# Optimization experiments

Measured on AMD Instinct MI355X. Metric: run time of the kernel, lower is better.

Reference implementation:

```python
import jax, jax.numpy as jnp
import numpy as np

N_P, N_A = 200_000, 100_000
D_P, D_A, H, OUT = 64, 64, 32, 1
E_PP, E_AP, E_PA = 3_200_000, 1_600_000, 1_600_000


def _lin(key, din, dout, bias=True):
    kw, kb = jax.random.split(key)
    W = jax.random.normal(kw, (din, dout), jnp.float32) * (1.0 / np.sqrt(din))
    if bias:
        b = jax.random.normal(kb, (dout,), jnp.float32) * 0.01
        return W, b
    return W


def setup_inputs() -> dict:
    key = jax.random.key(0)
    ks = jax.random.split(key, 24)
    inp = {}
    inp['x_paper'] = jax.random.normal(ks[0], (N_P, D_P), jnp.float32)
    inp['x_author'] = jax.random.normal(ks[1], (N_A, D_A), jnp.float32)
    inp['src_pp'] = jax.random.randint(ks[2], (E_PP,), 0, N_P)
    inp['dst_pp'] = jax.random.randint(ks[3], (E_PP,), 0, N_P)
    inp['src_ap'] = jax.random.randint(ks[4], (E_AP,), 0, N_A)
    inp['dst_ap'] = jax.random.randint(ks[5], (E_AP,), 0, N_P)
    inp['src_pa'] = jax.random.randint(ks[6], (E_PA,), 0, N_P)
    inp['dst_pa'] = jax.random.randint(ks[7], (E_PA,), 0, N_A)
    # Layer-1 SAGEConv weights per relation: lin_l (neighbor, with bias), lin_r (root, no bias)
    inp['Wl1_pp'], inp['bl1_pp'] = _lin(ks[8], D_P, H)
    inp['Wr1_pp'] = _lin(ks[9], D_P, H, bias=False)
    inp['Wl1_ap'], inp['bl1_ap'] = _lin(ks[10], D_A, H)
    inp['Wr1_ap'] = _lin(ks[11], D_P, H, bias=False)
    inp['Wl1_pa'], inp['bl1_pa'] = _lin(ks[12], D_P, H)
    inp['Wr1_pa'] = _lin(ks[13], D_A, H, bias=False)
    # Layer-2 SAGEConv weights (only relations feeding 'paper' affect the output)
    inp['Wl2_pp'], inp['bl2_pp'] = _lin(ks[14], H, H)
    inp['Wr2_pp'] = _lin(ks[15], H, H, bias=False)
    inp['Wl2_ap'], inp['bl2_ap'] = _lin(ks[16], H, H)
    inp['Wr2_ap'] = _lin(ks[17], H, H, bias=False)
    # Final classifier Linear(32, 1)
    inp['W_lin'], inp['b_lin'] = _lin(ks[18], H, OUT)
    return inp


def _sage_rel(x_src, x_dst, src, dst, Wl, bl, Wr):
    # SAGEConv: lin_l(mean_{j in N(i)} x_j) + lin_r(x_i)
    n_dst = x_dst.shape[0]
    agg = jax.ops.segment_sum(x_src[src], dst, num_segments=n_dst)
    cnt = jax.ops.segment_sum(jnp.ones((src.shape[0],), x_src.dtype), dst, num_segments=n_dst)
    mean = agg / jnp.maximum(cnt, 1.0)[:, None]
    return mean @ Wl + bl + x_dst @ Wr


def reference(x_paper, x_author, src_pp, dst_pp, src_ap, dst_ap, src_pa, dst_pa,
              Wl1_pp, bl1_pp, Wr1_pp, Wl1_ap, bl1_ap, Wr1_ap, Wl1_pa, bl1_pa, Wr1_pa,
              Wl2_pp, bl2_pp, Wr2_pp, Wl2_ap, bl2_ap, Wr2_ap, W_lin, b_lin):
    # Layer 1 (to_hetero: sum per-relation conv outputs per destination type), then relu
    p1 = (_sage_rel(x_paper, x_paper, src_pp, dst_pp, Wl1_pp, bl1_pp, Wr1_pp)
          + _sage_rel(x_author, x_paper, src_ap, dst_ap, Wl1_ap, bl1_ap, Wr1_ap))
    a1 = _sage_rel(x_paper, x_author, src_pa, dst_pa, Wl1_pa, bl1_pa, Wr1_pa)
    p1, a1 = jax.nn.relu(p1), jax.nn.relu(a1)
    # Layer 2: only 'paper' output is consumed downstream
    p2 = (_sage_rel(p1, p1, src_pp, dst_pp, Wl2_pp, bl2_pp, Wr2_pp)
          + _sage_rel(a1, p1, src_ap, dst_ap, Wl2_ap, bl2_ap, Wr2_ap))
    # model_config is None -> plain Linear, no sigmoid/softmax
    return p2 @ W_lin + b_lin
```

## Files before the change

kernel.cpp:

```cpp
#include <hip/hip_runtime.h>


typedef unsigned short ushort_t;
typedef __attribute__((ext_vector_type(8))) short bf16x8;
typedef __attribute__((ext_vector_type(4))) float f32x4;

#define PWBITS 9
#define PWIN   (1 << PWBITS)
#define PCHUNK 4096
#define CAPPAD 2048
#define FW_R   12

__device__ inline ushort_t f2bf(float f) {
    unsigned u = __float_as_uint(f);
    unsigned r = (u + 0x7FFFu + ((u >> 16) & 1u)) >> 16;
    return (ushort_t)r;
}
__device__ inline float bf2f_lo(unsigned u) { return __uint_as_float(u << 16); }
__device__ inline float bf2f_hi(unsigned u) { return __uint_as_float(u & 0xFFFF0000u); }
__device__ inline int ntl(const int* p) { return __builtin_nontemporal_load(p); }

__global__ void prep_weights(
    const float* __restrict__ Wl1_pp, const float* __restrict__ Wr1_pp,
    const float* __restrict__ Wl1_ap, const float* __restrict__ Wr1_ap,
    const float* __restrict__ Wl1_pa, const float* __restrict__ Wr1_pa,
    const float* __restrict__ bl1_pp, const float* __restrict__ bl1_ap,
    const float* __restrict__ bl1_pa,
    const float* __restrict__ Wl2_pp, const float* __restrict__ bl2_pp,
    const float* __restrict__ Wr2_pp,
    const float* __restrict__ Wl2_ap, const float* __restrict__ bl2_ap,
    const float* __restrict__ Wr2_ap,
    const float* __restrict__ W_lin, const float* __restrict__ b_lin,
    float* __restrict__ Wcomb_p,
    float* __restrict__ Wcomb_a,
    ushort_t* __restrict__ Wfrag_p,
    ushort_t* __restrict__ Wfrag_a,
    float* __restrict__ bias_p,
    float* __restrict__ bias_a,
    float* __restrict__ vv)
{
    int t = threadIdx.x;
    for (int idx = t; idx < 64 * 96; idx += 256) {
        int i = idx / 96, j = idx % 96;
        float v;
        if (j < 32)       v = Wl1_pp[i * 32 + j];
        else if (j < 64)  v = Wl1_pa[i * 32 + (j - 32)];
        else              v = Wr1_pp[i * 32 + (j - 64)] + Wr1_ap[i * 32 + (j - 64)];
        Wcomb_p[idx] = v;
    }
    for (int idx = t; idx < 64 * 64; idx += 256) {
        int i = idx / 64, j = idx % 64;
        Wcomb_a[idx] = (j < 32) ? Wl1_ap[i * 32 + j] : Wr1_pa[i * 32 + (j - 32)];
    }
    if (t < 32) {
        bias_p[t] = bl1_pp[t] + bl1_ap[t];
        bias_a[t] = bl1_pa[t];
        float vpp = 0.f, vr = 0.f, vap = 0.f;
        for (int j = 0; j < 32; ++j) {
            float wl = W_lin[j];
            vpp += Wl2_pp[t * 32 + j] * wl;
            vr  += (Wr2_pp[t * 32 + j] + Wr2_ap[t * 32 + j]) * wl;
            vap += Wl2_ap[t * 32 + j] * wl;
        }
        vv[t] = vpp; vv[32 + t] = vr; vv[96 + t] = vap;
    }
    if (t == 0) {
        float c = b_lin[0];
        for (int j = 0; j < 32; ++j) c += (bl2_pp[j] + bl2_ap[j]) * W_lin[j];
        vv[64] = c;
    }
    __syncthreads();
    for (int idx = t; idx < 12 * 64 * 8; idx += 256) {
        int f = idx >> 9, l = (idx >> 3) & 63, j = idx & 7;
        int nt = f >> 1, kh = f & 1;
        int k = kh * 32 + 8 * (l >> 4) + j;
        int n = nt * 16 + (l & 15);
        Wfrag_p[idx] = f2bf(Wcomb_p[k * 96 + n]);
    }
    for (int idx = t; idx < 8 * 64 * 8; idx += 256) {
        int f = idx >> 9, l = (idx >> 3) & 63, j = idx & 7;
        int nt = f >> 1, kh = f & 1;
        int k = kh * 32 + 8 * (l >> 4) + j;
        int n = nt * 16 + (l & 15);
        Wfrag_a[idx] = f2bf(Wcomb_a[k * 64 + n]);
    }
}

__global__ __launch_bounds__(256)
void partition3(
    const int* __restrict__ src0, const int* __restrict__ dst0, int E0,
    unsigned* __restrict__ bk0, int cap0, int nw0, int* __restrict__ wc0,
    const int* __restrict__ src1, const int* __restrict__ dst1, int E1,
    unsigned* __restrict__ bk1, int cap1, int nw1, int* __restrict__ wc1,
    const int* __restrict__ src2, const int* __restrict__ dst2, int E2,
    unsigned* __restrict__ bk2, int cap2, int nw2, int* __restrict__ wc2)
{
    __shared__ int lcnt[PWIN];
    __shared__ int lbase[PWIN];
    int nb0 = (E0 + PCHUNK - 1) / PCHUNK;
    int nb1 = (E1 + PCHUNK - 1) / PCHUNK;
    int b = blockIdx.x;
    const int* src; const int* dst; int E; unsigned* bk; int cap; int nw; int* wc; int chunk;
    if (b < nb0)            { src = src0; dst = dst0; E = E0; bk = bk0; cap = cap0; nw = nw0; wc = wc0; chunk = b; }
    else if (b < nb0 + nb1) { src = src1; dst = dst1; E = E1; bk = bk1; cap = cap1; nw = nw1; wc = wc1; chunk = b - nb0; }
    else                    { src = src2; dst = dst2; E = E2; bk = bk2; cap = cap2; nw = nw2; wc = wc2; chunk = b - nb0 - nb1; }
    int e0 = chunk * PCHUNK;
    int d_[16], s_[16];
#pragma unroll
    for (int r = 0; r < 4; ++r) {
        int base = e0 + r * 1024 + threadIdx.x * 4;
        if (base + 3 < E) {
            int4 dv = *(const int4*)(dst + base);
            int4 sv = *(const int4*)(src + base);
            d_[r * 4 + 0] = dv.x; d_[r * 4 + 1] = dv.y; d_[r * 4 + 2] = dv.z; d_[r * 4 + 3] = dv.w;
            s_[r * 4 + 0] = sv.x; s_[r * 4 + 1] = sv.y; s_[r * 4 + 2] = sv.z; s_[r * 4 + 3] = sv.w;
        } else {
#pragma unroll
            for (int k = 0; k < 4; ++k) {
                int e = base + k;
                d_[r * 4 + k] = (e < E) ? dst[e] : -1;
                s_[r * 4 + k] = 0;
            }
        }
    }
    for (int i = threadIdx.x; i < nw; i += 256) lcnt[i] = 0;
    __syncthreads();
#pragma unroll
    for (int k = 0; k < 16; ++k)
        if (d_[k] >= 0) atomicAdd(&lcnt[((unsigned)d_[k]) >> PWBITS], 1);
    __syncthreads();
    for (int i = threadIdx.x; i < nw; i += 256) {
        int c = lcnt[i];
        lbase[i] = (c > 0) ? atomicAdd(&wc[i * 16], c) : 0;
        lcnt[i] = 0;
    }
    __syncthreads();
#pragma unroll
    for (int k = 0; k < 16; ++k) {
        int d = d_[k];
        if (d >= 0) {
            int w = ((unsigned)d) >> PWBITS;
            int off = lbase[w] + atomicAdd(&lcnt[w], 1);
            if (off < cap)
                bk[(size_t)w * cap + off] =
                    (((unsigned)(d & (PWIN - 1))) << 18) | (unsigned)s_[k];
        }
    }
}

__global__ __launch_bounds__(256)
void fill_win3(
    const unsigned* __restrict__ bk0, const int* __restrict__ wc0, int cap0,
    int* __restrict__ csr0, int* __restrict__ cnt0, int* __restrict__ rs0, int N0, int nw0,
    const unsigned* __restrict__ bk1, const int* __restrict__ wc1, int cap1,
    int* __restrict__ csr1, int* __restrict__ cnt1, int* __restrict__ rs1, int N1, int nw1,
    const unsigned* __restrict__ bk2, const int* __restrict__ wc2, int cap2,
    int* __restrict__ csr2, int* __restrict__ cnt2, int* __restrict__ rs2, int N2, int nw2)
{
    __shared__ int lc[PWIN];
    __shared__ int wsum[4], wpre[4];
    int b = blockIdx.x;
    const unsigned* bk; const int* wc; int cap; int* csr; int* cnt; int* rs; int N; int w;
    if (b < nw0)            { bk = bk0; wc = wc0; cap = cap0; csr = csr0; cnt = cnt0; rs = rs0; N = N0; w = b; }
    else if (b < nw0 + nw1) { bk = bk1; wc = wc1; cap = cap1; csr = csr1; cnt = cnt1; rs = rs1; N = N1; w = b - nw0; }
    else                    { bk = bk2; wc = wc2; cap = cap2; csr = csr2; cnt = cnt2; rs = rs2; N = N2; w = b - nw0 - nw1; }
    int d0 = w << PWBITS;
    int sz = wc[w * 16]; if (sz > cap) sz = cap;
    const unsigned* bkt = bk + (size_t)w * cap;
    uint4 u[FW_R];
#pragma unroll
    for (int r = 0; r < FW_R; ++r) {
        int i4 = r * 1024 + threadIdx.x * 4;
        if (i4 + 3 < sz) {
            u[r] = *(const uint4*)(bkt + i4);
        } else {
            u[r].x = (i4 + 0 < sz) ? bkt[i4 + 0] : 0xFFFFFFFFu;
            u[r].y = (i4 + 1 < sz) ? bkt[i4 + 1] : 0xFFFFFFFFu;
            u[r].z = (i4 + 2 < sz) ? bkt[i4 + 2] : 0xFFFFFFFFu;
            u[r].w = (i4 + 3 < sz) ? bkt[i4 + 3] : 0xFFFFFFFFu;
        }
    }
    for (int i = threadIdx.x; i < PWIN; i += 256) lc[i] = 0;
    __syncthreads();
#pragma unroll
    for (int r = 0; r < FW_R; ++r) {
        if (u[r].x != 0xFFFFFFFFu) atomicAdd(&lc[u[r].x >> 18], 1);
        if (u[r].y != 0xFFFFFFFFu) atomicAdd(&lc[u[r].y >> 18], 1);
        if (u[r].z != 0xFFFFFFFFu) atomicAdd(&lc[u[r].z >> 18], 1);
        if (u[r].w != 0xFFFFFFFFu) atomicAdd(&lc[u[r].w >> 18], 1);
    }
    __syncthreads();
    {
        int i = threadIdx.x * 2;
        int d = d0 + i;
        if (d < N)     cnt[d] = lc[i];
        if (d + 1 < N) cnt[d + 1] = lc[i + 1];
    }
    int t2 = threadIdx.x * 2;
    int v0 = lc[t2], v1 = lc[t2 + 1];
    int ts = v0 + v1;
    int lane = threadIdx.x & 63;
    int wid = threadIdx.x >> 6;
    int incl = ts;
#pragma unroll
    for (int off = 1; off < 64; off <<= 1) {
        int o = __shfl_up(incl, off);
        if (lane >= off) incl += o;
    }
    if (lane == 63) wsum[wid] = incl;
    __syncthreads();
    if (threadIdx.x == 0) {
        int r = 0;
        for (int i = 0; i < 4; ++i) { wpre[i] = r; r += wsum[i]; }
    }
    __syncthreads();
    int run = w * cap + wpre[wid] + (incl - ts);
    lc[t2] = run;
    if (d0 + t2 < N) rs[d0 + t2] = run;
    run += v0;
    lc[t2 + 1] = run;
    if (d0 + t2 + 1 < N) rs[d0 + t2 + 1] = run;
    __syncthreads();
#pragma unroll
    for (int r = 0; r < FW_R; ++r) {
        if (u[r].x != 0xFFFFFFFFu) { int p = atomicAdd(&lc[u[r].x >> 18], 1); csr[p] = (int)(u[r].x & 0x3FFFFu); }
        if (u[r].y != 0xFFFFFFFFu) { int p = atomicAdd(&lc[u[r].y >> 18], 1); csr[p] = (int)(u[r].y & 0x3FFFFu); }
        if (u[r].z != 0xFFFFFFFFu) { int p = atomicAdd(&lc[u[r].z >> 18], 1); csr[p] = (int)(u[r].z & 0x3FFFFu); }
        if (u[r].w != 0xFFFFFFFFu) { int p = atomicAdd(&lc[u[r].w >> 18], 1); csr[p] = (int)(u[r].w & 0x3FFFFu); }
    }
}

__device__ inline bf16x8 cvt8(const float* p) {
    float4 a = *(const float4*)p;
    float4 b = *(const float4*)(p + 4);
    bf16x8 r;
    r[0] = (short)f2bf(a.x); r[1] = (short)f2bf(a.y);
    r[2] = (short)f2bf(a.z); r[3] = (short)f2bf(a.w);
    r[4] = (short)f2bf(b.x); r[5] = (short)f2bf(b.y);
    r[6] = (short)f2bf(b.z); r[7] = (short)f2bf(b.w);
    return r;
}

__global__ __launch_bounds__(256)
void proj_paper_mfma(const float* __restrict__ x, const ushort_t* __restrict__ Wfrag,
                     const float* __restrict__ bias,
                     ushort_t* __restrict__ h_pp, ushort_t* __restrict__ h_pa,
                     float* __restrict__ root_p, int N)
{
    int wave = threadIdx.x >> 6, lane = threadIdx.x & 63;
    int mbase = blockIdx.x * 64 + wave * 16;
    int row = lane & 15, grp = lane >> 4;
    int nA = mbase + row; if (nA > N - 1) nA = N - 1;
    const float* xr = x + (size_t)nA * 64 + grp * 8;
    bf16x8 a0 = cvt8(xr);
    bf16x8 a1 = cvt8(xr + 32);
    f32x4 acc0 = {0.f, 0.f, 0.f, 0.f}, acc1 = acc0, acc2 = acc0, acc3 = acc0;
    float bp0 = bias[row];
    float bp1 = bias[16 + row];
    f32x4 acc4 = {bp0, bp0, bp0, bp0};
    f32x4 acc5 = {bp1, bp1, bp1, bp1};
    const bf16x8* wf = (const bf16x8*)(Wfrag) + lane;
    acc0 = __builtin_amdgcn_mfma_f32_16x16x32_bf16(a0, wf[0 * 64], acc0, 0, 0, 0);
    acc0 = __builtin_amdgcn_mfma_f32_16x16x32_bf16(a1, wf[1 * 64], acc0, 0, 0, 0);
    acc1 = __builtin_amdgcn_mfma_f32_16x16x32_bf16(a0, wf[2 * 64], acc1, 0, 0, 0);
    acc1 = __builtin_amdgcn_mfma_f32_16x16x32_bf16(a1, wf[3 * 64], acc1, 0, 0, 0);
    acc2 = __builtin_amdgcn_mfma_f32_16x16x32_bf16(a0, wf[4 * 64], acc2, 0, 0, 0);
    acc2 = __builtin_amdgcn_mfma_f32_16x16x32_bf16(a1, wf[5 * 64], acc2, 0, 0, 0);
    acc3 = __builtin_amdgcn_mfma_f32_16x16x32_bf16(a0, wf[6 * 64], acc3, 0, 0, 0);
    acc3 = __builtin_amdgcn_mfma_f32_16x16x32_bf16(a1, wf[7 * 64], acc3, 0, 0, 0);
    acc4 = __builtin_amdgcn_mfma_f32_16x16x32_bf16(a0, wf[8 * 64], acc4, 0, 0, 0);
    acc4 = __builtin_amdgcn_mfma_f32_16x16x32_bf16(a1, wf[9 * 64], acc4, 0, 0, 0);
    acc5 = __builtin_amdgcn_mfma_f32_16x16x32_bf16(a0, wf[10 * 64], acc5, 0, 0, 0);
    acc5 = __builtin_amdgcn_mfma_f32_16x16x32_bf16(a1, wf[11 * 64], acc5, 0, 0, 0);
    int col = row;
    int node0 = mbase + grp * 4;
#pragma unroll
    for (int reg = 0; reg < 4; ++reg) {
        int nd = node0 + reg;
        if (nd < N) {
            size_t b32 = (size_t)nd * 32;
            h_pp[b32 + col]        = f2bf(acc0[reg]);
            h_pp[b32 + 16 + col]   = f2bf(acc1[reg]);
            h_pa[b32 + col]        = f2bf(acc2[reg]);
            h_pa[b32 + 16 + col]   = f2bf(acc3[reg]);
            root_p[b32 + col]      = acc4[reg];
            root_p[b32 + 16 + col] = acc5[reg];
        }
    }
}

__global__ __launch_bounds__(256)
void proj_author_mfma(const float* __restrict__ x, const ushort_t* __restrict__ Wfrag,
                      const float* __restrict__ bias,
                      ushort_t* __restrict__ h_ap, float* __restrict__ root_a, int N)
{
    int wave = threadIdx.x >> 6, lane = threadIdx.x & 63;
    int mbase = blockIdx.x * 64 + wave * 16;
    int row = lane & 15, grp = lane >> 4;
    int nA = mbase + row; if (nA > N - 1) nA = N - 1;
    const float* xr = x + (size_t)nA * 64 + grp * 8;
    bf16x8 a0 = cvt8(xr);
    bf16x8 a1 = cvt8(xr + 32);
    f32x4 acc0 = {0.f, 0.f, 0.f, 0.f}, acc1 = acc0;
    float bp0 = bias[row];
    float bp1 = bias[16 + row];
    f32x4 acc2 = {bp0, bp0, bp0, bp0};
    f32x4 acc3 = {bp1, bp1, bp1, bp1};
    const bf16x8* wf = (const bf16x8*)(Wfrag) + lane;
    acc0 = __builtin_amdgcn_mfma_f32_16x16x32_bf16(a0, wf[0 * 64], acc0, 0, 0, 0);
    acc0 = __builtin_amdgcn_mfma_f32_16x16x32_bf16(a1, wf[1 * 64], acc0, 0, 0, 0);
    acc1 = __builtin_amdgcn_mfma_f32_16x16x32_bf16(a0, wf[2 * 64], acc1, 0, 0, 0);
    acc1 = __builtin_amdgcn_mfma_f32_16x16x32_bf16(a1, wf[3 * 64], acc1, 0, 0, 0);
    acc2 = __builtin_amdgcn_mfma_f32_16x16x32_bf16(a0, wf[4 * 64], acc2, 0, 0, 0);
    acc2 = __builtin_amdgcn_mfma_f32_16x16x32_bf16(a1, wf[5 * 64], acc2, 0, 0, 0);
    acc3 = __builtin_amdgcn_mfma_f32_16x16x32_bf16(a0, wf[6 * 64], acc3, 0, 0, 0);
    acc3 = __builtin_amdgcn_mfma_f32_16x16x32_bf16(a1, wf[7 * 64], acc3, 0, 0, 0);
    int col = row;
    int node0 = mbase + grp * 4;
#pragma unroll
    for (int reg = 0; reg < 4; ++reg) {
        int nd = node0 + reg;
        if (nd < N) {
            size_t b32 = (size_t)nd * 32;
            h_ap[b32 + col]        = f2bf(acc0[reg]);
            h_ap[b32 + 16 + col]   = f2bf(acc1[reg]);
            root_a[b32 + col]      = acc2[reg];
            root_a[b32 + 16 + col] = acc3[reg];
        }
    }
}

#define ACC8(A, U) \
    A[0] += bf2f_lo((U).x); A[1] += bf2f_hi((U).x); \
    A[2] += bf2f_lo((U).y); A[3] += bf2f_hi((U).y); \
    A[4] += bf2f_lo((U).z); A[5] += bf2f_hi((U).z); \
    A[6] += bf2f_lo((U).w); A[7] += bf2f_hi((U).w);

__global__ __launch_bounds__(256, 8)
void pull_paper(const ushort_t* __restrict__ h_pp, const ushort_t* __restrict__ h_ap,
                const float* __restrict__ root,
                const int* __restrict__ csr_pp, const int* __restrict__ rs_pp,
                const int* __restrict__ cnt_pp,
                const int* __restrict__ csr_ap, const int* __restrict__ rs_ap,
                const int* __restrict__ cnt_ap,
                const float* __restrict__ vv,
                float* __restrict__ s_pp, float* __restrict__ out, int N)
{
    __shared__ float v0[32], v1[32];
    __shared__ float c2s;
    if (threadIdx.x < 32) { v0[threadIdx.x] = vv[threadIdx.x]; v1[threadIdx.x] = vv[32 + threadIdx.x]; }
    if (threadIdx.x == 0) c2s = vv[64];
    __syncthreads();
    int n = blockIdx.x * 64 + (threadIdx.x >> 2);
    if (n >= N) return;
    int c = threadIdx.x & 3;
    float a[8];
#pragma unroll
    for (int k = 0; k < 8; ++k) a[k] = 0.f;
    int s1 = rs_pp[n], k1 = cnt_pp[n], e1 = s1 + k1;
    int j = s1;
    for (; j + 4 <= e1; j += 4) {
        int i0 = ntl(csr_pp + j), i1 = ntl(csr_pp + j + 1);
        int i2 = ntl(csr_pp + j + 2), i3 = ntl(csr_pp + j + 3);
        uint4 u0 = ((const uint4*)(h_pp + (size_t)i0 * 32))[c];
        uint4 u1 = ((const uint4*)(h_pp + (size_t)i1 * 32))[c];
        uint4 u2 = ((const uint4*)(h_pp + (size_t)i2 * 32))[c];
        uint4 u3 = ((const uint4*)(h_pp + (size_t)i3 * 32))[c];
        ACC8(a, u0) ACC8(a, u1) ACC8(a, u2) ACC8(a, u3)
    }
    for (; j < e1; ++j) {
        uint4 u0 = ((const uint4*)(h_pp + (size_t)ntl(csr_pp + j) * 32))[c];
        ACC8(a, u0)
    }
    float b[8];
#pragma unroll
    for (int k = 0; k < 8; ++k) b[k] = 0.f;
    int s2 = rs_ap[n], k2 = cnt_ap[n], e2 = s2 + k2;
    j = s2;
    for (; j + 4 <= e2; j += 4) {
        int i0 = ntl(csr_ap + j), i1 = ntl(csr_ap + j + 1);
        int i2 = ntl(csr_ap + j + 2), i3 = ntl(csr_ap + j + 3);
        uint4 u0 = ((const uint4*)(h_ap + (size_t)i0 * 32))[c];
        uint4 u1 = ((const uint4*)(h_ap + (size_t)i1 * 32))[c];
        uint4 u2 = ((const uint4*)(h_ap + (size_t)i2 * 32))[c];
        uint4 u3 = ((const uint4*)(h_ap + (size_t)i3 * 32))[c];
        ACC8(b, u0) ACC8(b, u1) ACC8(b, u2) ACC8(b, u3)
    }
    for (; j < e2; ++j) {
        uint4 u0 = ((const uint4*)(h_ap + (size_t)ntl(csr_ap + j) * 32))[c];
        ACC8(b, u0)
    }
    float ipp = 1.0f / fmaxf((float)k1, 1.0f);
    float iap = 1.0f / fmaxf((float)k2, 1.0f);
    const float* rt = root + (size_t)n * 32 + 8 * c;
    float d0 = 0.f, d1 = 0.f;
#pragma unroll
    for (int k = 0; k < 8; ++k) {
        float p = fmaxf(rt[k] + a[k] * ipp + b[k] * iap, 0.f);
        d0 += p * v0[8 * c + k];
        d1 += p * v1[8 * c + k];
    }
    d0 += __shfl_xor(d0, 1); d0 += __shfl_xor(d0, 2);
    d1 += __shfl_xor(d1, 1); d1 += __shfl_xor(d1, 2);
    if (c == 0) { s_pp[n] = d0; out[n] = d1 + c2s; }
}

__global__ __launch_bounds__(256, 8)
void pull_author(const ushort_t* __restrict__ h_pa, const float* __restrict__ root,
                 const int* __restrict__ csr_pa, const int* __restrict__ rs_pa,
                 const int* __restrict__ cnt_pa,
                 const float* __restrict__ vv, float* __restrict__ s_ap, int N)
{
    __shared__ float v0[32];
    if (threadIdx.x < 32) v0[threadIdx.x] = vv[96 + threadIdx.x];
    __syncthreads();
    int n = blockIdx.x * 64 + (threadIdx.x >> 2);
    if (n >= N) return;
    int c = threadIdx.x & 3;
    float a[8];
#pragma unroll
    for (int k = 0; k < 8; ++k) a[k] = 0.f;
    int s1 = rs_pa[n], k1 = cnt_pa[n], e1 = s1 + k1;
    int j = s1;
    for (; j + 4 <= e1; j += 4) {
        int i0 = ntl(csr_pa + j), i1 = ntl(csr_pa + j + 1);
        int i2 = ntl(csr_pa + j + 2), i3 = ntl(csr_pa + j + 3);
        uint4 u0 = ((const uint4*)(h_pa + (size_t)i0 * 32))[c];
        uint4 u1 = ((const uint4*)(h_pa + (size_t)i1 * 32))[c];
        uint4 u2 = ((const uint4*)(h_pa + (size_t)i2 * 32))[c];
        uint4 u3 = ((const uint4*)(h_pa + (size_t)i3 * 32))[c];
        ACC8(a, u0) ACC8(a, u1) ACC8(a, u2) ACC8(a, u3)
    }
    for (; j < e1; ++j) {
        uint4 u0 = ((const uint4*)(h_pa + (size_t)ntl(csr_pa + j) * 32))[c];
        ACC8(a, u0)
    }
    float ip = 1.0f / fmaxf((float)k1, 1.0f);
    const float* rt = root + (size_t)n * 32 + 8 * c;
    float d0 = 0.f;
#pragma unroll
    for (int k = 0; k < 8; ++k) {
        float p = fmaxf(rt[k] + a[k] * ip, 0.f);
        d0 += p * v0[8 * c + k];
    }
    d0 += __shfl_xor(d0, 1); d0 += __shfl_xor(d0, 2);
    if (c == 0) s_ap[n] = d0;
}

__global__ __launch_bounds__(256, 8)
void pull2(const float* __restrict__ s_pp, const float* __restrict__ s_ap,
           const int* __restrict__ csr_pp, const int* __restrict__ rs_pp,
           const int* __restrict__ cnt_pp,
           const int* __restrict__ csr_ap, const int* __restrict__ rs_ap,
           const int* __restrict__ cnt_ap,
           float* __restrict__ out, int N)
{
    int g = (blockIdx.x * blockDim.x + threadIdx.x) >> 2;
    int c = threadIdx.x & 3;
    if (g >= N) return;
    int s1 = rs_pp[g], k1 = cnt_pp[g], e1 = s1 + k1;
    float t = 0.f;
    for (int j = s1 + c; j < e1; j += 4) t += s_pp[ntl(csr_pp + j)];
    int s2 = rs_ap[g], k2 = cnt_ap[g], e2 = s2 + k2;
    float u = 0.f;
    for (int j = s2 + c; j < e2; j += 4) u += s_ap[ntl(csr_ap + j)];
    t += __shfl_xor(t, 1); t += __shfl_xor(t, 2);
    u += __shfl_xor(u, 1); u += __shfl_xor(u, 2);
    if (c == 0) {
        out[g] += t / fmaxf((float)k1, 1.f) + u / fmaxf((float)k2, 1.f);
    }
}

extern "C" void kernel_launch(void* const* d_in, const int* in_sizes, int n_in,
                              void* d_out, int out_size, void* d_ws, size_t ws_size,
                              hipStream_t stream)
{
    const float* x_paper  = (const float*)d_in[0];
    const float* x_author = (const float*)d_in[1];
    const int* src_pp = (const int*)d_in[2];
    const int* dst_pp = (const int*)d_in[3];
    const int* src_ap = (const int*)d_in[4];
    const int* dst_ap = (const int*)d_in[5];
    const int* src_pa = (const int*)d_in[6];
    const int* dst_pa = (const int*)d_in[7];
    const float* Wl1_pp = (const float*)d_in[8];
    const float* bl1_pp = (const float*)d_in[9];
    const float* Wr1_pp = (const float*)d_in[10];
    const float* Wl1_ap = (const float*)d_in[11];
    const float* bl1_ap = (const float*)d_in[12];
    const float* Wr1_ap = (const float*)d_in[13];
    const float* Wl1_pa = (const float*)d_in[14];
    const float* bl1_pa = (const float*)d_in[15];
    const float* Wr1_pa = (const float*)d_in[16];
    const float* Wl2_pp = (const float*)d_in[17];
    const float* bl2_pp = (const float*)d_in[18];
    const float* Wr2_pp = (const float*)d_in[19];
    const float* Wl2_ap = (const float*)d_in[20];
    const float* bl2_ap = (const float*)d_in[21];
    const float* Wr2_ap = (const float*)d_in[22];
    const float* W_lin  = (const float*)d_in[23];
    const float* b_lin  = (const float*)d_in[24];

    const int NP = in_sizes[0] / 64;
    const int NA = in_sizes[1] / 64;
    const int E_PP = in_sizes[2];
    const int E_AP = in_sizes[4];
    const int E_PA = in_sizes[6];

    const int nw_pp = (NP + PWIN - 1) >> PWBITS;
    const int nw_ap = nw_pp;
    const int nw_pa = (NA + PWIN - 1) >> PWBITS;
    const int cap_pp = ((E_PP / nw_pp + CAPPAD) + 3) & ~3;
    const int cap_ap = ((E_AP / nw_ap + CAPPAD) + 3) & ~3;
    const int cap_pa = ((E_PA / nw_pa + CAPPAD) + 3) & ~3;

    char* wp = (char*)d_ws;
    int* wcur = (int*)wp;             wp += (size_t)3 * PWIN * 16 * 4;
    unsigned* bk_pp = (unsigned*)wp;  wp += (size_t)nw_pp * cap_pp * 4;
    unsigned* bk_ap = (unsigned*)wp;  wp += (size_t)nw_ap * cap_ap * 4;
    unsigned* bk_pa = (unsigned*)wp;  wp += (size_t)nw_pa * cap_pa * 4;
    int* csr_pp = (int*)wp;           wp += (size_t)nw_pp * cap_pp * 4;
    int* csr_ap = (int*)wp;           wp += (size_t)nw_ap * cap_ap * 4;
    int* csr_pa = (int*)wp;           wp += (size_t)nw_pa * cap_pa * 4;
    int* cnt    = (int*)wp;           wp += (size_t)(2 * NP + NA) * 4;
    int* rs     = (int*)wp;           wp += (size_t)(2 * NP + NA) * 4;
    ushort_t* h_pp = (ushort_t*)wp;   wp += (size_t)NP * 32 * 2;
    ushort_t* h_pa = (ushort_t*)wp;   wp += (size_t)NP * 32 * 2;
    ushort_t* h_ap = (ushort_t*)wp;   wp += (size_t)NA * 32 * 2;
    float* root_a = (float*)wp;       wp += (size_t)NA * 32 * 4;
    float* s_pp   = (float*)wp;       wp += (size_t)NP * 4;
    float* s_ap   = (float*)wp;       wp += (size_t)NA * 4;
    float* Wcomb_p = (float*)wp;      wp += 64 * 96 * 4;
    float* Wcomb_a = (float*)wp;      wp += 64 * 64 * 4;
    ushort_t* Wfrag_p = (ushort_t*)wp; wp += 12 * 64 * 8 * 2;
    ushort_t* Wfrag_a = (ushort_t*)wp; wp += 8 * 64 * 8 * 2;
    float* bias_p = (float*)wp;       wp += 32 * 4;
    float* bias_a = (float*)wp;       wp += 32 * 4;
    float* vv     = (float*)wp;       wp += 128 * 4;
    float* root_p = (float*)bk_pp;

    int* cnt_pp = cnt,  * cnt_ap = cnt + NP,  * cnt_pa = cnt + 2 * NP;
    int* rs_pp  = rs,   * rs_ap  = rs + NP,   * rs_pa  = rs + 2 * NP;

    float* out = (float*)d_out;

    hipMemsetAsync(wcur, 0, (size_t)3 * PWIN * 16 * 4, stream);

    prep_weights<<<1, 256, 0, stream>>>(
        Wl1_pp, Wr1_pp, Wl1_ap, Wr1_ap, Wl1_pa, Wr1_pa,
        bl1_pp, bl1_ap, bl1_pa,
        Wl2_pp, bl2_pp, Wr2_pp, Wl2_ap, bl2_ap, Wr2_ap,
        W_lin, b_lin, Wcomb_p, Wcomb_a, Wfrag_p, Wfrag_a, bias_p, bias_a, vv);

    int nb_total = (E_PP + PCHUNK - 1) / PCHUNK + (E_AP + PCHUNK - 1) / PCHUNK
                 + (E_PA + PCHUNK - 1) / PCHUNK;
    partition3<<<nb_total, 256, 0, stream>>>(
        src_pp, dst_pp, E_PP, bk_pp, cap_pp, nw_pp, wcur + 0,
        src_ap, dst_ap, E_AP, bk_ap, cap_ap, nw_ap, wcur + PWIN * 16,
        src_pa, dst_pa, E_PA, bk_pa, cap_pa, nw_pa, wcur + 2 * PWIN * 16);

    fill_win3<<<nw_pp + nw_ap + nw_pa, 256, 0, stream>>>(
        bk_pp, wcur + 0,            cap_pp, csr_pp, cnt_pp, rs_pp, NP, nw_pp,
        bk_ap, wcur + PWIN * 16,    cap_ap, csr_ap, cnt_ap, rs_ap, NP, nw_ap,
        bk_pa, wcur + 2 * PWIN * 16, cap_pa, csr_pa, cnt_pa, rs_pa, NA, nw_pa);

    proj_paper_mfma<<<(NP + 63) / 64, 256, 0, stream>>>(
        x_paper, Wfrag_p, bias_p, h_pp, h_pa, root_p, NP);
    proj_author_mfma<<<(NA + 63) / 64, 256, 0, stream>>>(
        x_author, Wfrag_a, bias_a, h_ap, root_a, NA);

    pull_paper<<<(NP + 63) / 64, 256, 0, stream>>>(
        h_pp, h_ap, root_p, csr_pp, rs_pp, cnt_pp, csr_ap, rs_ap, cnt_ap,
        vv, s_pp, out, NP);
    pull_author<<<(NA + 63) / 64, 256, 0, stream>>>(
        h_pa, root_a, csr_pa, rs_pa, cnt_pa, vv, s_ap, NA);

    pull2<<<((size_t)NP * 4 + 255) / 256, 256, 0, stream>>>(
        s_pp, s_ap, csr_pp, rs_pp, cnt_pp, csr_ap, rs_ap, cnt_ap, out, NP);
}
```

Measured before the change: 375.6 us.

## Fuse edge partition with node projection kernels into a single launch

```diff
diff --git a/kernel.cpp b/kernel.cpp
--- a/kernel.cpp
+++ b/kernel.cpp
@@ -31,12 +31,9 @@
     const float* __restrict__ Wl2_ap, const float* __restrict__ bl2_ap,
     const float* __restrict__ Wr2_ap,
     const float* __restrict__ W_lin, const float* __restrict__ b_lin,
-    float* __restrict__ Wcomb_p,
-    float* __restrict__ Wcomb_a,
-    ushort_t* __restrict__ Wfrag_p,
-    ushort_t* __restrict__ Wfrag_a,
-    float* __restrict__ bias_p,
-    float* __restrict__ bias_a,
+    float* __restrict__ Wcomb_p, float* __restrict__ Wcomb_a,
+    ushort_t* __restrict__ Wfrag_p, ushort_t* __restrict__ Wfrag_a,
+    float* __restrict__ bias_p, float* __restrict__ bias_a,
     float* __restrict__ vv)
 {
     int t = threadIdx.x;
@@ -86,20 +83,16 @@
     }
 }
 
-__global__ __launch_bounds__(256)
-void partition3(
+__device__ inline void partition_body(
+    int b, int nb0, int nb1,
     const int* __restrict__ src0, const int* __restrict__ dst0, int E0,
     unsigned* __restrict__ bk0, int cap0, int nw0, int* __restrict__ wc0,
     const int* __restrict__ src1, const int* __restrict__ dst1, int E1,
     unsigned* __restrict__ bk1, int cap1, int nw1, int* __restrict__ wc1,
     const int* __restrict__ src2, const int* __restrict__ dst2, int E2,
-    unsigned* __restrict__ bk2, int cap2, int nw2, int* __restrict__ wc2)
-{
-    __shared__ int lcnt[PWIN];
-    __shared__ int lbase[PWIN];
-    int nb0 = (E0 + PCHUNK - 1) / PCHUNK;
-    int nb1 = (E1 + PCHUNK - 1) / PCHUNK;
-    int b = blockIdx.x;
+    unsigned* __restrict__ bk2, int cap2, int nw2, int* __restrict__ wc2,
+    int* lcnt, int* lbase)
+{
     const int* src; const int* dst; int E; unsigned* bk; int cap; int nw; int* wc; int chunk;
     if (b < nb0)            { src = src0; dst = dst0; E = E0; bk = bk0; cap = cap0; nw = nw0; wc = wc0; chunk = b; }
     else if (b < nb0 + nb1) { src = src1; dst = dst1; E = E1; bk = bk1; cap = cap1; nw = nw1; wc = wc1; chunk = b - nb0; }
@@ -148,88 +141,6 @@
     }
 }
 
-__global__ __launch_bounds__(256)
-void fill_win3(
-    const unsigned* __restrict__ bk0, const int* __restrict__ wc0, int cap0,
-    int* __restrict__ csr0, int* __restrict__ cnt0, int* __restrict__ rs0, int N0, int nw0,
-    const unsigned* __restrict__ bk1, const int* __restrict__ wc1, int cap1,
-    int* __restrict__ csr1, int* __restrict__ cnt1, int* __restrict__ rs1, int N1, int nw1,
-    const unsigned* __restrict__ bk2, const int* __restrict__ wc2, int cap2,
-    int* __restrict__ csr2, int* __restrict__ cnt2, int* __restrict__ rs2, int N2, int nw2)
-{
-    __shared__ int lc[PWIN];
-    __shared__ int wsum[4], wpre[4];
-    int b = blockIdx.x;
-    const unsigned* bk; const int* wc; int cap; int* csr; int* cnt; int* rs; int N; int w;
-    if (b < nw0)            { bk = bk0; wc = wc0; cap = cap0; csr = csr0; cnt = cnt0; rs = rs0; N = N0; w = b; }
-    else if (b < nw0 + nw1) { bk = bk1; wc = wc1; cap = cap1; csr = csr1; cnt = cnt1; rs = rs1; N = N1; w = b - nw0; }
-    else                    { bk = bk2; wc = wc2; cap = cap2; csr = csr2; cnt = cnt2; rs = rs2; N = N2; w = b - nw0 - nw1; }
-    int d0 = w << PWBITS;
-    int sz = wc[w * 16]; if (sz > cap) sz = cap;
-    const unsigned* bkt = bk + (size_t)w * cap;
-    uint4 u[FW_R];
-#pragma unroll
-    for (int r = 0; r < FW_R; ++r) {
-        int i4 = r * 1024 + threadIdx.x * 4;
-        if (i4 + 3 < sz) {
-            u[r] = *(const uint4*)(bkt + i4);
-        } else {
-            u[r].x = (i4 + 0 < sz) ? bkt[i4 + 0] : 0xFFFFFFFFu;
-            u[r].y = (i4 + 1 < sz) ? bkt[i4 + 1] : 0xFFFFFFFFu;
-            u[r].z = (i4 + 2 < sz) ? bkt[i4 + 2] : 0xFFFFFFFFu;
-            u[r].w = (i4 + 3 < sz) ? bkt[i4 + 3] : 0xFFFFFFFFu;
-        }
-    }
-    for (int i = threadIdx.x; i < PWIN; i += 256) lc[i] = 0;
-    __syncthreads();
-#pragma unroll
-    for (int r = 0; r < FW_R; ++r) {
-        if (u[r].x != 0xFFFFFFFFu) atomicAdd(&lc[u[r].x >> 18], 1);
-        if (u[r].y != 0xFFFFFFFFu) atomicAdd(&lc[u[r].y >> 18], 1);
-        if (u[r].z != 0xFFFFFFFFu) atomicAdd(&lc[u[r].z >> 18], 1);
-        if (u[r].w != 0xFFFFFFFFu) atomicAdd(&lc[u[r].w >> 18], 1);
-    }
-    __syncthreads();
-    {
-        int i = threadIdx.x * 2;
-        int d = d0 + i;
-        if (d < N)     cnt[d] = lc[i];
-        if (d + 1 < N) cnt[d + 1] = lc[i + 1];
-    }
-    int t2 = threadIdx.x * 2;
-    int v0 = lc[t2], v1 = lc[t2 + 1];
-    int ts = v0 + v1;
-    int lane = threadIdx.x & 63;
-    int wid = threadIdx.x >> 6;
-    int incl = ts;
-#pragma unroll
-    for (int off = 1; off < 64; off <<= 1) {
-        int o = __shfl_up(incl, off);
-        if (lane >= off) incl += o;
-    }
-    if (lane == 63) wsum[wid] = incl;
-    __syncthreads();
-    if (threadIdx.x == 0) {
-        int r = 0;
-        for (int i = 0; i < 4; ++i) { wpre[i] = r; r += wsum[i]; }
-    }
-    __syncthreads();
-    int run = w * cap + wpre[wid] + (incl - ts);
-    lc[t2] = run;
-    if (d0 + t2 < N) rs[d0 + t2] = run;
-    run += v0;
-    lc[t2 + 1] = run;
-    if (d0 + t2 + 1 < N) rs[d0 + t2 + 1] = run;
-    __syncthreads();
-#pragma unroll
-    for (int r = 0; r < FW_R; ++r) {
-        if (u[r].x != 0xFFFFFFFFu) { int p = atomicAdd(&lc[u[r].x >> 18], 1); csr[p] = (int)(u[r].x & 0x3FFFFu); }
-        if (u[r].y != 0xFFFFFFFFu) { int p = atomicAdd(&lc[u[r].y >> 18], 1); csr[p] = (int)(u[r].y & 0x3FFFFu); }
-        if (u[r].z != 0xFFFFFFFFu) { int p = atomicAdd(&lc[u[r].z >> 18], 1); csr[p] = (int)(u[r].z & 0x3FFFFu); }
-        if (u[r].w != 0xFFFFFFFFu) { int p = atomicAdd(&lc[u[r].w >> 18], 1); csr[p] = (int)(u[r].w & 0x3FFFFu); }
-    }
-}
-
 __device__ inline bf16x8 cvt8(const float* p) {
     float4 a = *(const float4*)p;
     float4 b = *(const float4*)(p + 4);
@@ -241,14 +152,14 @@
     return r;
 }
 
-__global__ __launch_bounds__(256)
-void proj_paper_mfma(const float* __restrict__ x, const ushort_t* __restrict__ Wfrag,
-                     const float* __restrict__ bias,
-                     ushort_t* __restrict__ h_pp, ushort_t* __restrict__ h_pa,
-                     float* __restrict__ root_p, int N)
+__device__ inline void proj_paper_body(
+    int blk, const float* __restrict__ x, const ushort_t* __restrict__ Wfrag,
+    const float* __restrict__ bias,
+    ushort_t* __restrict__ h_pp, ushort_t* __restrict__ h_pa,
+    float* __restrict__ root_p, int N)
 {
     int wave = threadIdx.x >> 6, lane = threadIdx.x & 63;
-    int mbase = blockIdx.x * 64 + wave * 16;
+    int mbase = blk * 64 + wave * 16;
     int row = lane & 15, grp = lane >> 4;
     int nA = mbase + row; if (nA > N - 1) nA = N - 1;
     const float* xr = x + (size_t)nA * 64 + grp * 8;
@@ -272,30 +183,29 @@
     acc4 = __builtin_amdgcn_mfma_f32_16x16x32_bf16(a1, wf[9 * 64], acc4, 0, 0, 0);
     acc5 = __builtin_amdgcn_mfma_f32_16x16x32_bf16(a0, wf[10 * 64], acc5, 0, 0, 0);
     acc5 = __builtin_amdgcn_mfma_f32_16x16x32_bf16(a1, wf[11 * 64], acc5, 0, 0, 0);
-    int col = row;
     int node0 = mbase + grp * 4;
 #pragma unroll
     for (int reg = 0; reg < 4; ++reg) {
         int nd = node0 + reg;
         if (nd < N) {
             size_t b32 = (size_t)nd * 32;
-            h_pp[b32 + col]        = f2bf(acc0[reg]);
-            h_pp[b32 + 16 + col]   = f2bf(acc1[reg]);
-            h_pa[b32 + col]        = f2bf(acc2[reg]);
-            h_pa[b32 + 16 + col]   = f2bf(acc3[reg]);
-            root_p[b32 + col]      = acc4[reg];
-            root_p[b32 + 16 + col] = acc5[reg];
+            h_pp[b32 + row]        = f2bf(acc0[reg]);
+            h_pp[b32 + 16 + row]   = f2bf(acc1[reg]);
+            h_pa[b32 + row]        = f2bf(acc2[reg]);
+            h_pa[b32 + 16 + row]   = f2bf(acc3[reg]);
+            root_p[b32 + row]      = acc4[reg];
+            root_p[b32 + 16 + row] = acc5[reg];
         }
     }
 }
 
-__global__ __launch_bounds__(256)
-void proj_author_mfma(const float* __restrict__ x, const ushort_t* __restrict__ Wfrag,
-                      const float* __restrict__ bias,
-                      ushort_t* __restrict__ h_ap, float* __restrict__ root_a, int N)
+__device__ inline void proj_author_body(
+    int blk, const float* __restrict__ x, const ushort_t* __restrict__ Wfrag,
+    const float* __restrict__ bias,
+    ushort_t* __restrict__ h_ap, float* __restrict__ root_a, int N)
 {
     int wave = threadIdx.x >> 6, lane = threadIdx.x & 63;
-    int mbase = blockIdx.x * 64 + wave * 16;
+    int mbase = blk * 64 + wave * 16;
     int row = lane & 15, grp = lane >> 4;
     int nA = mbase + row; if (nA > N - 1) nA = N - 1;
     const float* xr = x + (size_t)nA * 64 + grp * 8;
@@ -315,18 +225,166 @@
     acc2 = __builtin_amdgcn_mfma_f32_16x16x32_bf16(a1, wf[5 * 64], acc2, 0, 0, 0);
     acc3 = __builtin_amdgcn_mfma_f32_16x16x32_bf16(a0, wf[6 * 64], acc3, 0, 0, 0);
     acc3 = __builtin_amdgcn_mfma_f32_16x16x32_bf16(a1, wf[7 * 64], acc3, 0, 0, 0);
-    int col = row;
     int node0 = mbase + grp * 4;
 #pragma unroll
     for (int reg = 0; reg < 4; ++reg) {
         int nd = node0 + reg;
         if (nd < N) {
             size_t b32 = (size_t)nd * 32;
-            h_ap[b32 + col]        = f2bf(acc0[reg]);
-            h_ap[b32 + 16 + col]   = f2bf(acc1[reg]);
-            root_a[b32 + col]      = acc2[reg];
-            root_a[b32 + 16 + col] = acc3[reg];
+            h_ap[b32 + row]        = f2bf(acc0[reg]);
+            h_ap[b32 + 16 + row]   = f2bf(acc1[reg]);
+            root_a[b32 + row]      = acc2[reg];
+            root_a[b32 + 16 + row] = acc3[reg];
         }
+    }
+}
+
+__global__ __launch_bounds__(256)
+void part_proj(
+    const int* __restrict__ src0, const int* __restrict__ dst0, int E0,
+    unsigned* __restrict__ bk0, int cap0, int nw0, int* __restrict__ wc0,
+    const int* __restrict__ src1, const int* __restrict__ dst1, int E1,
+    unsigned* __restrict__ bk1, int cap1, int nw1, int* __restrict__ wc1,
+    const int* __restrict__ src2, const int* __restrict__ dst2, int E2,
+    unsigned* __restrict__ bk2, int cap2, int nw2, int* __restrict__ wc2,
+    const float* __restrict__ xp, const float* __restrict__ xa,
+    const ushort_t* __restrict__ Wfp, const ushort_t* __restrict__ Wfa,
+    const float* __restrict__ bias_p, const float* __restrict__ bias_a,
+    ushort_t* __restrict__ h_pp, ushort_t* __restrict__ h_pa,
+    ushort_t* __restrict__ h_ap,
+    float* __restrict__ root_p, float* __restrict__ root_a,
+    int NP, int NA, int nbt, int pbp)
+{
+    __shared__ int lcnt[PWIN];
+    __shared__ int lbase[PWIN];
+    int b = blockIdx.x;
+    int nb0 = (E0 + PCHUNK - 1) / PCHUNK;
+    int nb1 = (E1 + PCHUNK - 1) / PCHUNK;
+    if (b < nbt) {
+        partition_body(b, nb0, nb1,
+                       src0, dst0, E0, bk0, cap0, nw0, wc0,
+                       src1, dst1, E1, bk1, cap1, nw1, wc1,
+                       src2, dst2, E2, bk2, cap2, nw2, wc2, lcnt, lbase);
+    } else if (b < nbt + pbp) {
+        proj_paper_body(b - nbt, xp, Wfp, bias_p, h_pp, h_pa, root_p, NP);
+    } else {
+        proj_author_body(b - nbt - pbp, xa, Wfa, bias_a, h_ap, root_a, NA);
+    }
+}
+
+__global__ __launch_bounds__(256)
+void partition3(
+    const int* __restrict__ src0, const int* __restrict__ dst0, int E0,
+    unsigned* __restrict__ bk0, int cap0, int nw0, int* __restrict__ wc0,
+    const int* __restrict__ src1, const int* __restrict__ dst1, int E1,
+    unsigned* __restrict__ bk1, int cap1, int nw1, int* __restrict__ wc1,
+    const int* __restrict__ src2, const int* __restrict__ dst2, int E2,
+    unsigned* __restrict__ bk2, int cap2, int nw2, int* __restrict__ wc2)
+{
+    __shared__ int lcnt[PWIN];
+    __shared__ int lbase[PWIN];
+    int nb0 = (E0 + PCHUNK - 1) / PCHUNK;
+    int nb1 = (E1 + PCHUNK - 1) / PCHUNK;
+    partition_body(blockIdx.x, nb0, nb1,
+                   src0, dst0, E0, bk0, cap0, nw0, wc0,
+                   src1, dst1, E1, bk1, cap1, nw1, wc1,
+                   src2, dst2, E2, bk2, cap2, nw2, wc2, lcnt, lbase);
+}
+
+__global__ __launch_bounds__(256)
+void proj_all(const float* __restrict__ xp, const float* __restrict__ xa,
+              const ushort_t* __restrict__ Wfp, const ushort_t* __restrict__ Wfa,
+              const float* __restrict__ bias_p, const float* __restrict__ bias_a,
+              ushort_t* __restrict__ h_pp, ushort_t* __restrict__ h_pa,
+              ushort_t* __restrict__ h_ap,
+              float* __restrict__ root_p, float* __restrict__ root_a,
+              int NP, int NA, int pbp)
+{
+    if (blockIdx.x < pbp)
+        proj_paper_body(blockIdx.x, xp, Wfp, bias_p, h_pp, h_pa, root_p, NP);
+    else
+        proj_author_body(blockIdx.x - pbp, xa, Wfa, bias_a, h_ap, root_a, NA);
+}
+
+__global__ __launch_bounds__(256)
+void fill_win3(
+    const unsigned* __restrict__ bk0, const int* __restrict__ wc0, int cap0,
+    int* __restrict__ csr0, int* __restrict__ cnt0, int* __restrict__ rs0, int N0, int nw0,
+    const unsigned* __restrict__ bk1, const int* __restrict__ wc1, int cap1,
+    int* __restrict__ csr1, int* __restrict__ cnt1, int* __restrict__ rs1, int N1, int nw1,
+    const unsigned* __restrict__ bk2, const int* __restrict__ wc2, int cap2,
+    int* __restrict__ csr2, int* __restrict__ cnt2, int* __restrict__ rs2, int N2, int nw2)
+{
+    __shared__ int lc[PWIN];
+    __shared__ int wsum[4], wpre[4];
+    int b = blockIdx.x;
+    const unsigned* bk; const int* wc; int cap; int* csr; int* cnt; int* rs; int N; int w;
+    if (b < nw0)            { bk = bk0; wc = wc0; cap = cap0; csr = csr0; cnt = cnt0; rs = rs0; N = N0; w = b; }
+    else if (b < nw0 + nw1) { bk = bk1; wc = wc1; cap = cap1; csr = csr1; cnt = cnt1; rs = rs1; N = N1; w = b - nw0; }
+    else                    { bk = bk2; wc = wc2; cap = cap2; csr = csr2; cnt = cnt2; rs = rs2; N = N2; w = b - nw0 - nw1; }
+    int d0 = w << PWBITS;
+    int sz = wc[w * 16]; if (sz > cap) sz = cap;
+    const unsigned* bkt = bk + (size_t)w * cap;
+    uint4 u[FW_R];
+#pragma unroll
+    for (int r = 0; r < FW_R; ++r) {
+        int i4 = r * 1024 + threadIdx.x * 4;
+        if (i4 + 3 < sz) {
+            u[r] = *(const uint4*)(bkt + i4);
+        } else {
+            u[r].x = (i4 + 0 < sz) ? bkt[i4 + 0] : 0xFFFFFFFFu;
+            u[r].y = (i4 + 1 < sz) ? bkt[i4 + 1] : 0xFFFFFFFFu;
+            u[r].z = (i4 + 2 < sz) ? bkt[i4 + 2] : 0xFFFFFFFFu;
+            u[r].w = (i4 + 3 < sz) ? bkt[i4 + 3] : 0xFFFFFFFFu;
+        }
+    }
+    for (int i = threadIdx.x; i < PWIN; i += 256) lc[i] = 0;
+    __syncthreads();
+#pragma unroll
+    for (int r = 0; r < FW_R; ++r) {
+        if (u[r].x != 0xFFFFFFFFu) atomicAdd(&lc[u[r].x >> 18], 1);
+        if (u[r].y != 0xFFFFFFFFu) atomicAdd(&lc[u[r].y >> 18], 1);
+        if (u[r].z != 0xFFFFFFFFu) atomicAdd(&lc[u[r].z >> 18], 1);
+        if (u[r].w != 0xFFFFFFFFu) atomicAdd(&lc[u[r].w >> 18], 1);
+    }
+    __syncthreads();
+    {
+        int i = threadIdx.x * 2;
+        int d = d0 + i;
+        if (d < N)     cnt[d] = lc[i];
+        if (d + 1 < N) cnt[d + 1] = lc[i + 1];
+    }
+    int t2 = threadIdx.x * 2;
+    int v0 = lc[t2], v1 = lc[t2 + 1];
+    int ts = v0 + v1;
+    int lane = threadIdx.x & 63;
+    int wid = threadIdx.x >> 6;
+    int incl = ts;
+#pragma unroll
+    for (int off = 1; off < 64; off <<= 1) {
+        int o = __shfl_up(incl, off);
+        if (lane >= off) incl += o;
+    }
+    if (lane == 63) wsum[wid] = incl;
+    __syncthreads();
+    if (threadIdx.x == 0) {
+        int r = 0;
+        for (int i = 0; i < 4; ++i) { wpre[i] = r; r += wsum[i]; }
+    }
+    __syncthreads();
+    int run = w * cap + wpre[wid] + (incl - ts);
+    lc[t2] = run;
+    if (d0 + t2 < N) rs[d0 + t2] = run;
+    run += v0;
+    lc[t2 + 1] = run;
+    if (d0 + t2 + 1 < N) rs[d0 + t2 + 1] = run;
+    __syncthreads();
+#pragma unroll
+    for (int r = 0; r < FW_R; ++r) {
+        if (u[r].x != 0xFFFFFFFFu) { int p = atomicAdd(&lc[u[r].x >> 18], 1); csr[p] = (int)(u[r].x & 0x3FFFFu); }
+        if (u[r].y != 0xFFFFFFFFu) { int p = atomicAdd(&lc[u[r].y >> 18], 1); csr[p] = (int)(u[r].y & 0x3FFFFu); }
+        if (u[r].z != 0xFFFFFFFFu) { int p = atomicAdd(&lc[u[r].z >> 18], 1); csr[p] = (int)(u[r].z & 0x3FFFFu); }
+        if (u[r].w != 0xFFFFFFFFu) { int p = atomicAdd(&lc[u[r].w >> 18], 1); csr[p] = (int)(u[r].w & 0x3FFFFu); }
     }
 }
 
@@ -537,7 +595,10 @@
     float* bias_p = (float*)wp;       wp += 32 * 4;
     float* bias_a = (float*)wp;       wp += 32 * 4;
     float* vv     = (float*)wp;       wp += 128 * 4;
-    float* root_p = (float*)bk_pp;
+    size_t used = (size_t)(wp - (char*)d_ws);
+    size_t rootp_bytes = (size_t)NP * 32 * 4;
+    bool fused = (used + rootp_bytes) <= ws_size;
+    float* root_p = fused ? (float*)wp : (float*)bk_pp;
 
     int* cnt_pp = cnt,  * cnt_ap = cnt + NP,  * cnt_pa = cnt + 2 * NP;
     int* rs_pp  = rs,   * rs_ap  = rs + NP,   * rs_pa  = rs + 2 * NP;
@@ -554,20 +615,36 @@
 
     int nb_total = (E_PP + PCHUNK - 1) / PCHUNK + (E_AP + PCHUNK - 1) / PCHUNK
                  + (E_PA + PCHUNK - 1) / PCHUNK;
-    partition3<<<nb_total, 256, 0, stream>>>(
-        src_pp, dst_pp, E_PP, bk_pp, cap_pp, nw_pp, wcur + 0,
-        src_ap, dst_ap, E_AP, bk_ap, cap_ap, nw_ap, wcur + PWIN * 16,
-        src_pa, dst_pa, E_PA, bk_pa, cap_pa, nw_pa, wcur + 2 * PWIN * 16);
-
-    fill_win3<<<nw_pp + nw_ap + nw_pa, 256, 0, stream>>>(
-        bk_pp, wcur + 0,            cap_pp, csr_pp, cnt_pp, rs_pp, NP, nw_pp,
-        bk_ap, wcur + PWIN * 16,    cap_ap, csr_ap, cnt_ap, rs_ap, NP, nw_ap,
-        bk_pa, wcur + 2 * PWIN * 16, cap_pa, csr_pa, cnt_pa, rs_pa, NA, nw_pa);
-
-    proj_paper_mfma<<<(NP + 63) / 64, 256, 0, stream>>>(
-        x_paper, Wfrag_p, bias_p, h_pp, h_pa, root_p, NP);
-    proj_author_mfma<<<(NA + 63) / 64, 256, 0, stream>>>(
-        x_author, Wfrag_a, bias_a, h_ap, root_a, NA);
+    int pbp = (NP + 63) / 64;
+    int pba = (NA + 63) / 64;
+
+    if (fused) {
+        part_proj<<<nb_total + pbp + pba, 256, 0, stream>>>(
+            src_pp, dst_pp, E_PP, bk_pp, cap_pp, nw_pp, wcur + 0,
+            src_ap, dst_ap, E_AP, bk_ap, cap_ap, nw_ap, wcur + PWIN * 16,
+            src_pa, dst_pa, E_PA, bk_pa, cap_pa, nw_pa, wcur + 2 * PWIN * 16,
+            x_paper, x_author, Wfrag_p, Wfrag_a, bias_p, bias_a,
+            h_pp, h_pa, h_ap, root_p, root_a, NP, NA, nb_total, pbp);
+
+        fill_win3<<<nw_pp + nw_ap + nw_pa, 256, 0, stream>>>(
+            bk_pp, wcur + 0,             cap_pp, csr_pp, cnt_pp, rs_pp, NP, nw_pp,
+            bk_ap, wcur + PWIN * 16,     cap_ap, csr_ap, cnt_ap, rs_ap, NP, nw_ap,
+            bk_pa, wcur + 2 * PWIN * 16, cap_pa, csr_pa, cnt_pa, rs_pa, NA, nw_pa);
+    } else {
+        partition3<<<nb_total, 256, 0, stream>>>(
+            src_pp, dst_pp, E_PP, bk_pp, cap_pp, nw_pp, wcur + 0,
+            src_ap, dst_ap, E_AP, bk_ap, cap_ap, nw_ap, wcur + PWIN * 16,
+            src_pa, dst_pa, E_PA, bk_pa, cap_pa, nw_pa, wcur + 2 * PWIN * 16);
+
+        fill_win3<<<nw_pp + nw_ap + nw_pa, 256, 0, stream>>>(
+            bk_pp, wcur + 0,             cap_pp, csr_pp, cnt_pp, rs_pp, NP, nw_pp,
+            bk_ap, wcur + PWIN * 16,     cap_ap, csr_ap, cnt_ap, rs_ap, NP, nw_ap,
+            bk_pa, wcur + 2 * PWIN * 16, cap_pa, csr_pa, cnt_pa, rs_pa, NA, nw_pa);
+
+        proj_all<<<pbp + pba, 256, 0, stream>>>(
+            x_paper, x_author, Wfrag_p, Wfrag_a, bias_p, bias_a,
+            h_pp, h_pa, h_ap, root_p, root_a, NP, NA, pbp);
+    }
 
     pull_paper<<<(NP + 63) / 64, 256, 0, stream>>>(
         h_pp, h_ap, root_p, csr_pp, rs_pp, cnt_pp, csr_ap, rs_ap, cnt_ap,
```

New measurement: 367.6 us. 1.02x faster.
